# Optimization experiments

Measured on AMD Instinct MI355X. Metric: run time of the kernel, lower is better.

Reference implementation:

```python
import jax, jax.numpy as jnp
import numpy as np

TEMPERATURE = 8.0  # sqrt(d_k) with d_k = 64
NEG_INF = -jnp.inf


def setup_inputs() -> dict:
    key = jax.random.key(0)
    kq, kk, kv = jax.random.split(key, 3)
    b, n, d = 16, 2048, 64
    q = jax.random.normal(kq, (b, n, d), dtype=jnp.float32)
    k = jax.random.normal(kk, (b, n, d), dtype=jnp.float32)
    v = jax.random.normal(kv, (b, n, d), dtype=jnp.float32)
    # causal mask: True where attention is disallowed (strict upper triangle)
    mask = jnp.broadcast_to(jnp.triu(jnp.ones((n, n), dtype=bool), k=1), (b, n, n))
    return {"q": q, "k": k, "v": v, "mask": mask}


def reference(q, k, v, mask):
    # attn = q @ k^T / temperature   [b, n, n]
    attn = jnp.einsum('bqd,bkd->bqk', q, k) / TEMPERATURE
    attn = jnp.where(mask, NEG_INF, attn)
    attn = jax.nn.softmax(attn, axis=2)
    # output = attn @ v   [b, n, d]
    output = jnp.einsum('bqk,bkd->bqd', attn, v)
    return (output, attn)
```

## Files before the change

### kernel.cpp

```cpp
#include <hip/hip_runtime.h>


constexpr int B = 16;
constexpr int N = 2048;
constexpr int D = 64;
constexpr float INV_TEMP = 0.125f;
constexpr size_t QK_ELEMS = (size_t)B * N * D;

typedef __attribute__((ext_vector_type(8))) short bf16x8;
typedef __attribute__((ext_vector_type(4))) float f32x4;

__device__ __forceinline__ short f2bf(float f) {
    __bf16 h = (__bf16)f;
    return __builtin_bit_cast(short, h);
}

__global__ __launch_bounds__(256) void sdpa_convert(
    const float* __restrict__ q, const float* __restrict__ k, const float* __restrict__ v,
    short* __restrict__ qbf, short* __restrict__ kbf, short* __restrict__ vt)
{
    const int blk = blockIdx.x;
    const int t = threadIdx.x;
    if (blk < 512) {
        __shared__ short sT[64][72];
        const int b = blk >> 5, n0 = (blk & 31) * 64;
        const int srow = t >> 2, sd = (t & 3) * 16;
        const float4* src = (const float4*)(v + ((size_t)b * N + n0 + srow) * D + sd);
        float4 f0 = src[0], f1 = src[1], f2 = src[2], f3 = src[3];
        float vals[16] = {f0.x,f0.y,f0.z,f0.w, f1.x,f1.y,f1.z,f1.w,
                          f2.x,f2.y,f2.z,f2.w, f3.x,f3.y,f3.z,f3.w};
        short* dst = &sT[srow][sd];
#pragma unroll
        for (int i = 0; i < 16; ++i) dst[i] = f2bf(vals[i]);
        __syncthreads();
        const int d = t >> 2, nc = (t & 3) * 16;
        bf16x8 o0, o1;
#pragma unroll
        for (int i = 0; i < 8; ++i) o0[i] = sT[nc + i][d];
#pragma unroll
        for (int i = 0; i < 8; ++i) o1[i] = sT[nc + 8 + i][d];
        short* dstv = vt + ((size_t)b * D + d) * N + n0 + nc;
        *(bf16x8*)dstv = o0;
        *(bf16x8*)(dstv + 8) = o1;
    } else {
        size_t gi = (size_t)(blk - 512) * 2048 + (size_t)t * 8;
        const float* src; short* dst;
        if (gi < QK_ELEMS) { src = q + gi;             dst = qbf + gi; }
        else               { src = k + (gi - QK_ELEMS); dst = kbf + (gi - QK_ELEMS); }
        float4 f0 = ((const float4*)src)[0];
        float4 f1 = ((const float4*)src)[1];
        bf16x8 o;
        o[0]=f2bf(f0.x); o[1]=f2bf(f0.y); o[2]=f2bf(f0.z); o[3]=f2bf(f0.w);
        o[4]=f2bf(f1.x); o[5]=f2bf(f1.y); o[6]=f2bf(f1.z); o[7]=f2bf(f1.w);
        *(bf16x8*)dst = o;
    }
}

__global__ __launch_bounds__(256) void sdpa_main(
    const short* __restrict__ qbf, const short* __restrict__ kbf, const short* __restrict__ vt,
    float* __restrict__ out, float* __restrict__ attn)
{
    const int x = blockIdx.x;
    const int b = x >> 5;
    const int u = x & 31;
    const int qt = (u & 1) ? (31 - (u >> 1)) : (u >> 1);
    const int qs = qt * 64;

    const int t    = threadIdx.x;
    const int w    = t >> 6;
    const int lane = t & 63;
    const int l15  = lane & 15;
    const int quad = lane >> 4;
    const int q8   = quad * 8;

    __shared__ __align__(16) short sP[4][16][72];

    const short* kb  = kbf + (size_t)b * N * D;
    const short* vtb = vt  + (size_t)b * D * N;
    float* attn_b = attn + (size_t)b * N * N;

    {
        const int srow = t >> 2;
        const int ce = (qt + 1) * 64;
        float4 z = {0.f, 0.f, 0.f, 0.f};
        float* arow = attn_b + (size_t)(qs + srow) * N;
        for (int c = ce + (t & 3) * 16; c < N; c += 64) {
            float4* p4 = (float4*)(arow + c);
            p4[0] = z; p4[1] = z; p4[2] = z; p4[3] = z;
        }
    }

    const short* qrow = qbf + ((size_t)b * N + qs + w * 16 + l15) * D;
    const bf16x8 qa0 = *(const bf16x8*)(qrow + q8);
    const bf16x8 qa1 = *(const bf16x8*)(qrow + 32 + q8);

    float rs[4] = {0.f, 0.f, 0.f, 0.f};
    for (int kt = 0; kt <= qt; ++kt) {
        const bool diag = (kt == qt);
#pragma unroll
        for (int nt = 0; nt < 4; ++nt) {
            const short* krow = kb + (size_t)(kt * 64 + nt * 16 + l15) * D;
            bf16x8 b0 = *(const bf16x8*)(krow + q8);
            bf16x8 b1 = *(const bf16x8*)(krow + 32 + q8);
            f32x4 c = {0.f, 0.f, 0.f, 0.f};
            c = __builtin_amdgcn_mfma_f32_16x16x32_bf16(qa0, b0, c, 0, 0, 0);
            c = __builtin_amdgcn_mfma_f32_16x16x32_bf16(qa1, b1, c, 0, 0, 0);
            const int col = nt * 16 + l15;
#pragma unroll
            for (int r = 0; r < 4; ++r) {
                const int rowl = w * 16 + quad * 4 + r;
                rs[r] += (!diag || col <= rowl) ? __expf(c[r] * INV_TEMP) : 0.f;
            }
        }
    }
    float inv[4];
#pragma unroll
    for (int r = 0; r < 4; ++r) {
        float s = rs[r];
        s += __shfl_xor(s, 1);
        s += __shfl_xor(s, 2);
        s += __shfl_xor(s, 4);
        s += __shfl_xor(s, 8);
        inv[r] = 1.f / s;
    }

    f32x4 o[4];
#pragma unroll
    for (int nt = 0; nt < 4; ++nt) o[nt] = (f32x4){0.f, 0.f, 0.f, 0.f};

    for (int kt = 0; kt <= qt; ++kt) {
        const bool diag = (kt == qt);
#pragma unroll
        for (int nt = 0; nt < 4; ++nt) {
            const short* krow = kb + (size_t)(kt * 64 + nt * 16 + l15) * D;
            bf16x8 b0 = *(const bf16x8*)(krow + q8);
            bf16x8 b1 = *(const bf16x8*)(krow + 32 + q8);
            f32x4 c = {0.f, 0.f, 0.f, 0.f};
            c = __builtin_amdgcn_mfma_f32_16x16x32_bf16(qa0, b0, c, 0, 0, 0);
            c = __builtin_amdgcn_mfma_f32_16x16x32_bf16(qa1, b1, c, 0, 0, 0);
            const int col = nt * 16 + l15;
            float* arow = attn_b + (size_t)(qs + w * 16 + quad * 4) * N + kt * 64 + col;
#pragma unroll
            for (int r = 0; r < 4; ++r) {
                const int rowl = w * 16 + quad * 4 + r;
                float p = (!diag || col <= rowl) ? __expf(c[r] * INV_TEMP) * inv[r] : 0.f;
                arow[(size_t)r * N] = p;
                sP[w][quad * 4 + r][col] = f2bf(p);
            }
        }
#pragma unroll
        for (int kc = 0; kc < 2; ++kc) {
            bf16x8 a = *(const bf16x8*)&sP[w][l15][kc * 32 + q8];
#pragma unroll
            for (int nt = 0; nt < 4; ++nt) {
                const short* vrow = vtb + (size_t)(nt * 16 + l15) * N + kt * 64 + kc * 32 + q8;
                bf16x8 vf = *(const bf16x8*)vrow;
                o[nt] = __builtin_amdgcn_mfma_f32_16x16x32_bf16(a, vf, o[nt], 0, 0, 0);
            }
        }
    }

#pragma unroll
    for (int nt = 0; nt < 4; ++nt) {
        float* orow = out + ((size_t)(b * N + qs + w * 16 + quad * 4)) * D + nt * 16 + l15;
#pragma unroll
        for (int r = 0; r < 4; ++r) orow[(size_t)r * D] = o[nt][r];
    }
}

extern "C" void kernel_launch(void* const* d_in, const int* in_sizes, int n_in,
                              void* d_out, int out_size, void* d_ws, size_t ws_size,
                              hipStream_t stream) {
    const float* q = (const float*)d_in[0];
    const float* k = (const float*)d_in[1];
    const float* v = (const float*)d_in[2];

    float* out  = (float*)d_out;
    float* attn = out + (size_t)B * N * D;

    short* qbf = (short*)d_ws;
    short* kbf = qbf + QK_ELEMS;
    short* vtb = kbf + QK_ELEMS;

    sdpa_convert<<<dim3(2560), dim3(256), 0, stream>>>(q, k, v, qbf, kbf, vtb);
    sdpa_main<<<dim3(B * 32), dim3(256), 0, stream>>>(qbf, kbf, vtb, out, attn);
}
```

Before: 551.2 us.

## Split attention along key dimension into rowsum, write, and reduce kernels

Replaces the single per-query-tile main kernel, which had only 512 blocks of very uneven causal work, with a split-K scheme. Each query tile is divided into up to 8 chunks of 256 keys. Row sums are accumulated atomically, a write kernel emits the normalized probabilities and partial outputs per chunk, and a final kernel sums the partial outputs. The aim is more parallelism and better load balance across CUs for the bandwidth-bound attn write. In exchange it adds kernel launches, atomics, and a partial-output buffer that must be written and read back.

```diff
diff --git a/kernel.cpp b/kernel.cpp
--- a/kernel.cpp
+++ b/kernel.cpp
@@ -17,7 +17,8 @@
 
 __global__ __launch_bounds__(256) void sdpa_convert(
     const float* __restrict__ q, const float* __restrict__ k, const float* __restrict__ v,
-    short* __restrict__ qbf, short* __restrict__ kbf, short* __restrict__ vt)
+    short* __restrict__ qbf, short* __restrict__ kbf, short* __restrict__ vt,
+    float* __restrict__ rsum)
 {
     const int blk = blockIdx.x;
     const int t = threadIdx.x;
@@ -42,10 +43,10 @@
         short* dstv = vt + ((size_t)b * D + d) * N + n0 + nc;
         *(bf16x8*)dstv = o0;
         *(bf16x8*)(dstv + 8) = o1;
-    } else {
+    } else if (blk < 2560) {
         size_t gi = (size_t)(blk - 512) * 2048 + (size_t)t * 8;
         const float* src; short* dst;
-        if (gi < QK_ELEMS) { src = q + gi;             dst = qbf + gi; }
+        if (gi < QK_ELEMS) { src = q + gi;              dst = qbf + gi; }
         else               { src = k + (gi - QK_ELEMS); dst = kbf + (gi - QK_ELEMS); }
         float4 f0 = ((const float4*)src)[0];
         float4 f1 = ((const float4*)src)[1];
@@ -53,67 +54,54 @@
         o[0]=f2bf(f0.x); o[1]=f2bf(f0.y); o[2]=f2bf(f0.z); o[3]=f2bf(f0.w);
         o[4]=f2bf(f1.x); o[5]=f2bf(f1.y); o[6]=f2bf(f1.z); o[7]=f2bf(f1.w);
         *(bf16x8*)dst = o;
-    }
-}
-
-__global__ __launch_bounds__(256) void sdpa_main(
-    const short* __restrict__ qbf, const short* __restrict__ kbf, const short* __restrict__ vt,
-    float* __restrict__ out, float* __restrict__ attn)
-{
-    const int x = blockIdx.x;
-    const int b = x >> 5;
-    const int u = x & 31;
-    const int qt = (u & 1) ? (31 - (u >> 1)) : (u >> 1);
+    } else {
+        int idx = ((blk - 2560) * 256 + t) * 4;
+        float4 z = {0.f, 0.f, 0.f, 0.f};
+        *(float4*)(rsum + idx) = z;
+    }
+}
+
+__global__ __launch_bounds__(256) void sdpa_rowsum(
+    const short* __restrict__ qbf, const short* __restrict__ kbf,
+    float* __restrict__ rsum)
+{
+    const int blk = blockIdx.x;
+    const int b  = blk >> 8;
+    const int qt = (blk >> 3) & 31;
+    const int c  = blk & 7;
+    const int nch = (qt + 4) >> 2;
+    if (c >= nch) return;
     const int qs = qt * 64;
 
-    const int t    = threadIdx.x;
-    const int w    = t >> 6;
-    const int lane = t & 63;
-    const int l15  = lane & 15;
-    const int quad = lane >> 4;
-    const int q8   = quad * 8;
-
-    __shared__ __align__(16) short sP[4][16][72];
-
-    const short* kb  = kbf + (size_t)b * N * D;
-    const short* vtb = vt  + (size_t)b * D * N;
-    float* attn_b = attn + (size_t)b * N * N;
-
-    {
-        const int srow = t >> 2;
-        const int ce = (qt + 1) * 64;
-        float4 z = {0.f, 0.f, 0.f, 0.f};
-        float* arow = attn_b + (size_t)(qs + srow) * N;
-        for (int c = ce + (t & 3) * 16; c < N; c += 64) {
-            float4* p4 = (float4*)(arow + c);
-            p4[0] = z; p4[1] = z; p4[2] = z; p4[3] = z;
-        }
-    }
+    const int t = threadIdx.x;
+    const int w = t >> 6, lane = t & 63, l15 = lane & 15, quad = lane >> 4, q8 = quad * 8;
 
     const short* qrow = qbf + ((size_t)b * N + qs + w * 16 + l15) * D;
     const bf16x8 qa0 = *(const bf16x8*)(qrow + q8);
     const bf16x8 qa1 = *(const bf16x8*)(qrow + 32 + q8);
+    const short* kb = kbf + (size_t)b * N * D;
 
     float rs[4] = {0.f, 0.f, 0.f, 0.f};
-    for (int kt = 0; kt <= qt; ++kt) {
+    const int kt0 = c * 4;
+    const int kte = min(qt, kt0 + 3);
+    for (int kt = kt0; kt <= kte; ++kt) {
         const bool diag = (kt == qt);
 #pragma unroll
         for (int nt = 0; nt < 4; ++nt) {
             const short* krow = kb + (size_t)(kt * 64 + nt * 16 + l15) * D;
             bf16x8 b0 = *(const bf16x8*)(krow + q8);
             bf16x8 b1 = *(const bf16x8*)(krow + 32 + q8);
-            f32x4 c = {0.f, 0.f, 0.f, 0.f};
-            c = __builtin_amdgcn_mfma_f32_16x16x32_bf16(qa0, b0, c, 0, 0, 0);
-            c = __builtin_amdgcn_mfma_f32_16x16x32_bf16(qa1, b1, c, 0, 0, 0);
+            f32x4 cc = {0.f, 0.f, 0.f, 0.f};
+            cc = __builtin_amdgcn_mfma_f32_16x16x32_bf16(qa0, b0, cc, 0, 0, 0);
+            cc = __builtin_amdgcn_mfma_f32_16x16x32_bf16(qa1, b1, cc, 0, 0, 0);
             const int col = nt * 16 + l15;
 #pragma unroll
             for (int r = 0; r < 4; ++r) {
                 const int rowl = w * 16 + quad * 4 + r;
-                rs[r] += (!diag || col <= rowl) ? __expf(c[r] * INV_TEMP) : 0.f;
-            }
-        }
-    }
-    float inv[4];
+                rs[r] += (!diag || col <= rowl) ? __expf(cc[r] * INV_TEMP) : 0.f;
+            }
+        }
+    }
 #pragma unroll
     for (int r = 0; r < 4; ++r) {
         float s = rs[r];
@@ -121,30 +109,81 @@
         s += __shfl_xor(s, 2);
         s += __shfl_xor(s, 4);
         s += __shfl_xor(s, 8);
-        inv[r] = 1.f / s;
-    }
+        if (l15 == 0) atomicAdd(&rsum[b * N + qs + w * 16 + quad * 4 + r], s);
+    }
+}
+
+__global__ __launch_bounds__(256) void sdpa_write(
+    const short* __restrict__ qbf, const short* __restrict__ kbf,
+    const short* __restrict__ vt, const float* __restrict__ rsum,
+    float* __restrict__ attn, float* __restrict__ pout)
+{
+    const int blk = blockIdx.x;
+    const int b  = blk >> 8;
+    const int qt = (blk >> 3) & 31;
+    const int c  = blk & 7;
+    const int qs = qt * 64;
+    const int nch = (qt + 4) >> 2;
+    const int t = threadIdx.x;
+    float* attn_b = attn + (size_t)b * N * N;
+
+    if (c >= nch) {
+        const int row = t >> 2;
+        float4 z = {0.f, 0.f, 0.f, 0.f};
+        float* base = attn_b + (size_t)(qs + row) * N + c * 256 + (t & 3) * 16;
+#pragma unroll
+        for (int j = 0; j < 4; ++j) {
+            float4* p4 = (float4*)(base + j * 64);
+            p4[0] = z; p4[1] = z; p4[2] = z; p4[3] = z;
+        }
+        return;
+    }
+
+    const int w = t >> 6, lane = t & 63, l15 = lane & 15, quad = lane >> 4, q8 = quad * 8;
+    __shared__ __align__(16) short sP[4][16][72];
+
+    const short* qrow = qbf + ((size_t)b * N + qs + w * 16 + l15) * D;
+    const bf16x8 qa0 = *(const bf16x8*)(qrow + q8);
+    const bf16x8 qa1 = *(const bf16x8*)(qrow + 32 + q8);
+    const short* kb  = kbf + (size_t)b * N * D;
+    const short* vtb = vt  + (size_t)b * D * N;
+
+    float inv[4];
+#pragma unroll
+    for (int r = 0; r < 4; ++r)
+        inv[r] = 1.f / rsum[b * N + qs + w * 16 + quad * 4 + r];
 
     f32x4 o[4];
 #pragma unroll
     for (int nt = 0; nt < 4; ++nt) o[nt] = (f32x4){0.f, 0.f, 0.f, 0.f};
 
-    for (int kt = 0; kt <= qt; ++kt) {
+    for (int i = 0; i < 4; ++i) {
+        const int kt = c * 4 + i;
+        float* arow = attn_b + (size_t)(qs + w * 16 + quad * 4) * N + kt * 64;
+        if (kt > qt) {
+#pragma unroll
+            for (int nt = 0; nt < 4; ++nt) {
+                const int col = nt * 16 + l15;
+#pragma unroll
+                for (int r = 0; r < 4; ++r) arow[(size_t)r * N + col] = 0.f;
+            }
+            continue;
+        }
         const bool diag = (kt == qt);
 #pragma unroll
         for (int nt = 0; nt < 4; ++nt) {
             const short* krow = kb + (size_t)(kt * 64 + nt * 16 + l15) * D;
             bf16x8 b0 = *(const bf16x8*)(krow + q8);
             bf16x8 b1 = *(const bf16x8*)(krow + 32 + q8);
-            f32x4 c = {0.f, 0.f, 0.f, 0.f};
-            c = __builtin_amdgcn_mfma_f32_16x16x32_bf16(qa0, b0, c, 0, 0, 0);
-            c = __builtin_amdgcn_mfma_f32_16x16x32_bf16(qa1, b1, c, 0, 0, 0);
+            f32x4 cc = {0.f, 0.f, 0.f, 0.f};
+            cc = __builtin_amdgcn_mfma_f32_16x16x32_bf16(qa0, b0, cc, 0, 0, 0);
+            cc = __builtin_amdgcn_mfma_f32_16x16x32_bf16(qa1, b1, cc, 0, 0, 0);
             const int col = nt * 16 + l15;
-            float* arow = attn_b + (size_t)(qs + w * 16 + quad * 4) * N + kt * 64 + col;
 #pragma unroll
             for (int r = 0; r < 4; ++r) {
                 const int rowl = w * 16 + quad * 4 + r;
-                float p = (!diag || col <= rowl) ? __expf(c[r] * INV_TEMP) * inv[r] : 0.f;
-                arow[(size_t)r * N] = p;
+                float p = (!diag || col <= rowl) ? __expf(cc[r] * INV_TEMP) * inv[r] : 0.f;
+                arow[(size_t)r * N + col] = p;
                 sP[w][quad * 4 + r][col] = f2bf(p);
             }
         }
@@ -160,11 +199,34 @@
         }
     }
 
+    float* pbase = pout + (size_t)blk * 4096;
 #pragma unroll
     for (int nt = 0; nt < 4; ++nt) {
-        float* orow = out + ((size_t)(b * N + qs + w * 16 + quad * 4)) * D + nt * 16 + l15;
-#pragma unroll
-        for (int r = 0; r < 4; ++r) orow[(size_t)r * D] = o[nt][r];
+        const int col = nt * 16 + l15;
+#pragma unroll
+        for (int r = 0; r < 4; ++r)
+            pbase[(w * 16 + quad * 4 + r) * 64 + col] = o[nt][r];
+    }
+}
+
+__global__ __launch_bounds__(256) void sdpa_oreduce(
+    const float* __restrict__ pout, float* __restrict__ out)
+{
+    const int blk = blockIdx.x;
+    const int b = blk >> 5, qt = blk & 31, qs = qt * 64;
+    const int nch = (qt + 4) >> 2;
+    const int t = threadIdx.x;
+    const float* base = pout + (size_t)blk * 8 * 4096;
+#pragma unroll
+    for (int j = 0; j < 4; ++j) {
+        const int e = t * 16 + j * 4;
+        float4 s = {0.f, 0.f, 0.f, 0.f};
+        for (int cc = 0; cc < nch; ++cc) {
+            float4 v = *(const float4*)(base + (size_t)cc * 4096 + e);
+            s.x += v.x; s.y += v.y; s.z += v.z; s.w += v.w;
+        }
+        const int row = e >> 6, d = e & 63;
+        *(float4*)(out + ((size_t)(b * N + qs + row)) * D + d) = s;
     }
 }
 
@@ -178,10 +240,14 @@
     float* out  = (float*)d_out;
     float* attn = out + (size_t)B * N * D;
 
-    short* qbf = (short*)d_ws;
-    short* kbf = qbf + QK_ELEMS;
-    short* vtb = kbf + QK_ELEMS;
-
-    sdpa_convert<<<dim3(2560), dim3(256), 0, stream>>>(q, k, v, qbf, kbf, vtb);
-    sdpa_main<<<dim3(B * 32), dim3(256), 0, stream>>>(qbf, kbf, vtb, out, attn);
-}
+    short* qbf  = (short*)d_ws;
+    short* kbf  = qbf + QK_ELEMS;
+    short* vtb  = kbf + QK_ELEMS;
+    float* rsum = (float*)(vtb + QK_ELEMS);
+    float* pout = rsum + (size_t)B * N;
+
+    sdpa_convert<<<dim3(2592), dim3(256), 0, stream>>>(q, k, v, qbf, kbf, vtb, rsum);
+    sdpa_rowsum<<<dim3(4096), dim3(256), 0, stream>>>(qbf, kbf, rsum);
+    sdpa_write<<<dim3(4096), dim3(256), 0, stream>>>(qbf, kbf, vtb, rsum, attn, pout);
+    sdpa_oreduce<<<dim3(512), dim3(256), 0, stream>>>(pout, out);
+}
```

After: 572.0 us. 3.8% more time.
